# Optimization experiments

Hardware: AMD Instinct MI355X
Metric: run time of the kernel (lower is better)

Reference implementation:

```python
import jax, jax.numpy as jnp
import numpy as np

B = 4194304
RAD2DEG = 180.0 / np.pi


def setup_inputs() -> dict:
    key = jax.random.key(0)
    k1, k2, k3 = jax.random.split(key, 3)
    label = jax.random.normal(k1, (B, 3, 2), dtype=jnp.float32)
    est_label = jax.random.normal(k2, (B, 6), dtype=jnp.float32)
    mix_way = jax.random.randint(k3, (B,), 0, 2, dtype=jnp.int32)  # 0='single', 1=mixed
    return {"label": label, "est_label": est_label, "mix_way": mix_way}


def reference(label, est_label, mix_way):
    # --- permutation-invariant MSE loss ---
    e1, e2 = est_label[:, :3], est_label[:, 3:]            # [B,3] each
    l1, l2 = label[:, :, 0], label[:, :, 1]                 # [B,3] each
    mse = lambda a, b: jnp.mean((a - b) ** 2, axis=-1)      # per-batch mean over 3 comps
    loss_perm1 = mse(e1, l1) + mse(e2, l2)                  # [B]
    loss_perm2 = mse(e2, l1) + mse(e1, l2)                  # [B]
    mixed_loss = jnp.minimum(loss_perm1, loss_perm2)        # [B]
    # 'single' branch in the original uses the FULL (unindexed) tensors -> same scalar each time
    single_loss = jnp.mean((est_label[:, :3] - label[:, :, 0]) ** 2)
    per_batch = jnp.where(mix_way == 0, single_loss, mixed_loss)
    label_loss = jnp.mean(per_batch)

    # --- azimuth MAE with angle wrap-around and best pairing ---
    lab_az1 = jnp.arctan2(label[:, 1, 0], label[:, 0, 0]) * RAD2DEG
    lab_az2 = jnp.arctan2(label[:, 1, 1], label[:, 0, 1]) * RAD2DEG
    est_az1 = jnp.arctan2(est_label[:, 1], est_label[:, 0]) * RAD2DEG
    est_az2 = jnp.arctan2(est_label[:, 4], est_label[:, 3]) * RAD2DEG

    def wrap(e):
        e = jnp.abs(e)
        return jnp.where(e > 180.0, 360.0 - e, e)

    e11 = wrap(lab_az1 - est_az1)
    e22 = wrap(lab_az2 - est_az2)
    e12 = wrap(lab_az1 - est_az2)
    e21 = wrap(lab_az2 - est_az1)

    use_direct = (e11 + e22) < (e12 + e21)
    mae1 = jnp.mean(jnp.where(use_direct, e11, e12))
    mae2 = jnp.mean(jnp.where(use_direct, e22, e21))

    return (label_loss, mae1, mae2)
```

## Files before the change

### kernel.cpp

```cpp
#include <hip/hip_runtime.h>
#include <math.h>

#define RAD2DEG 57.29577951308232f

constexpr int S1_BLOCKS = 2048;
constexpr int S1_TPB    = 256;

__device__ __forceinline__ float wrapdeg(float e) {
    e = fabsf(e);
    return e > 180.0f ? 360.0f - e : e;
}

__device__ __forceinline__ void per_row(
    float l1x, float l2x, float l1y, float l2y, float l1z, float l2z,
    float e1x, float e1y, float e1z, float e2x, float e2y, float e2z,
    int mw,
    float& sS, float& sM, float& sC0, float& sM1, float& sM2)
{
    float dx, dy, dz;
    dx = e1x - l1x; dy = e1y - l1y; dz = e1z - l1z;
    float d11 = dx*dx + dy*dy + dz*dz;
    dx = e2x - l2x; dy = e2y - l2y; dz = e2z - l2z;
    float d22 = dx*dx + dy*dy + dz*dz;
    dx = e2x - l1x; dy = e2y - l1y; dz = e2z - l1z;
    float d21 = dx*dx + dy*dy + dz*dz;
    dx = e1x - l2x; dy = e1y - l2y; dz = e1z - l2z;
    float d12 = dx*dx + dy*dy + dz*dz;

    sS += d11;

    float mixed = fminf(d11 + d22, d21 + d12) * (1.0f / 3.0f);
    if (mw != 0) sM += mixed; else sC0 += 1.0f;

    float la1 = atan2f(l1y, l1x) * RAD2DEG;
    float la2 = atan2f(l2y, l2x) * RAD2DEG;
    float ea1 = atan2f(e1y, e1x) * RAD2DEG;
    float ea2 = atan2f(e2y, e2x) * RAD2DEG;

    float e11 = wrapdeg(la1 - ea1);
    float e22 = wrapdeg(la2 - ea2);
    float e12 = wrapdeg(la1 - ea2);
    float e21 = wrapdeg(la2 - ea1);

    bool ud = (e11 + e22) < (e12 + e21);
    sM1 += ud ? e11 : e12;
    sM2 += ud ? e22 : e21;
}

__global__ __launch_bounds__(S1_TPB) void stage1_kernel(
    const float* __restrict__ label,
    const float* __restrict__ est,
    const int*   __restrict__ mix,
    float* __restrict__ partials,
    int P)
{
    const int tid = threadIdx.x;
    const int gid = blockIdx.x * S1_TPB + tid;
    const int T   = gridDim.x * S1_TPB;

    float sS = 0.f, sM = 0.f, sC0 = 0.f, sM1 = 0.f, sM2 = 0.f;

    for (int p = gid; p < P; p += T) {
        const float4* lab4 = (const float4*)(label + (size_t)p * 12);
        const float4* est4 = (const float4*)(est   + (size_t)p * 12);
        float4 L0 = lab4[0], L1 = lab4[1], L2 = lab4[2];
        float4 E0 = est4[0], E1 = est4[1], E2 = est4[2];
        int2 mw = ((const int2*)mix)[p];

        per_row(L0.x, L0.y, L0.z, L0.w, L1.x, L1.y,
                E0.x, E0.y, E0.z, E0.w, E1.x, E1.y,
                mw.x, sS, sM, sC0, sM1, sM2);
        per_row(L1.z, L1.w, L2.x, L2.y, L2.z, L2.w,
                E1.z, E1.w, E2.x, E2.y, E2.z, E2.w,
                mw.y, sS, sM, sC0, sM1, sM2);
    }

    for (int off = 32; off > 0; off >>= 1) {
        sS  += __shfl_down(sS,  off, 64);
        sM  += __shfl_down(sM,  off, 64);
        sC0 += __shfl_down(sC0, off, 64);
        sM1 += __shfl_down(sM1, off, 64);
        sM2 += __shfl_down(sM2, off, 64);
    }

    __shared__ float red[S1_TPB / 64][5];
    const int wid = tid >> 6, lane = tid & 63;
    if (lane == 0) {
        red[wid][0] = sS; red[wid][1] = sM; red[wid][2] = sC0;
        red[wid][3] = sM1; red[wid][4] = sM2;
    }
    __syncthreads();
    if (tid == 0) {
        float r0 = 0.f, r1 = 0.f, r2 = 0.f, r3 = 0.f, r4 = 0.f;
        #pragma unroll
        for (int w = 0; w < S1_TPB / 64; ++w) {
            r0 += red[w][0]; r1 += red[w][1]; r2 += red[w][2];
            r3 += red[w][3]; r4 += red[w][4];
        }
        float* out = partials + (size_t)blockIdx.x * 5;
        out[0] = r0; out[1] = r1; out[2] = r2; out[3] = r3; out[4] = r4;
    }
}

__global__ __launch_bounds__(256) void stage2_kernel(
    const float* __restrict__ partials,
    float* __restrict__ out,
    int nblocks,
    long long Btot)
{
    const int tid = threadIdx.x;
    double aS = 0, aM = 0, aC0 = 0, aM1 = 0, aM2 = 0;
    for (int r = tid; r < nblocks; r += 256) {
        const float* row = partials + (size_t)r * 5;
        aS += row[0]; aM += row[1]; aC0 += row[2]; aM1 += row[3]; aM2 += row[4];
    }
    for (int off = 32; off > 0; off >>= 1) {
        aS  += __shfl_down(aS,  off, 64);
        aM  += __shfl_down(aM,  off, 64);
        aC0 += __shfl_down(aC0, off, 64);
        aM1 += __shfl_down(aM1, off, 64);
        aM2 += __shfl_down(aM2, off, 64);
    }
    __shared__ double red[4][5];
    const int wid = tid >> 6, lane = tid & 63;
    if (lane == 0) {
        red[wid][0] = aS; red[wid][1] = aM; red[wid][2] = aC0;
        red[wid][3] = aM1; red[wid][4] = aM2;
    }
    __syncthreads();
    if (tid == 0) {
        double S = 0, M = 0, C0 = 0, M1 = 0, M2 = 0;
        #pragma unroll
        for (int w = 0; w < 4; ++w) {
            S += red[w][0]; M += red[w][1]; C0 += red[w][2];
            M1 += red[w][3]; M2 += red[w][4];
        }
        const double Bd = (double)Btot;
        const double single_loss = S / (3.0 * Bd);
        out[0] = (float)((C0 * single_loss + M) / Bd);
        out[1] = (float)(M1 / Bd);
        out[2] = (float)(M2 / Bd);
    }
}

extern "C" void kernel_launch(void* const* d_in, const int* in_sizes, int n_in,
                              void* d_out, int out_size, void* d_ws, size_t ws_size,
                              hipStream_t stream) {
    const float* label = (const float*)d_in[0];
    const float* est   = (const float*)d_in[1];
    const int*   mix   = (const int*)d_in[2];
    float* out = (float*)d_out;
    float* partials = (float*)d_ws;

    const long long B = (long long)in_sizes[2];
    const int P = (int)(B / 2);

    stage1_kernel<<<S1_BLOCKS, S1_TPB, 0, stream>>>(label, est, mix, partials, P);
    stage2_kernel<<<1, 256, 0, stream>>>(partials, out, S1_BLOCKS, B);
}
```

Baseline: 233.2 us.

## Compute wrapped azimuth differences directly via dot/cross polynomial atan

Replaces four atan2f calls and the wrap-around subtraction with a direct angle-between-vectors computation. It uses the dot and cross products of each label/estimate pair, a fast reciprocal and a minimax atan polynomial. This removes the expensive libm atan2 paths, though it now evaluates four angle computations instead of four atan2 calls. The mix-way branch is also turned into a branchless multiply. It risks small accuracy differences from the polynomial and the approximate reciprocal.

```diff
diff --git a/kernel.cpp b/kernel.cpp
--- a/kernel.cpp
+++ b/kernel.cpp
@@ -6,9 +6,24 @@
 constexpr int S1_BLOCKS = 2048;
 constexpr int S1_TPB    = 256;
 
-__device__ __forceinline__ float wrapdeg(float e) {
-    e = fabsf(e);
-    return e > 180.0f ? 360.0f - e : e;
+__device__ __forceinline__ float angdist_deg(float ax, float ay,
+                                             float bx, float by) {
+    float dot = ax * bx + ay * by;
+    float cr  = fabsf(ay * bx - ax * by);
+    float ad  = fabsf(dot);
+    float mn  = fminf(cr, ad);
+    float mx  = fmaxf(cr, ad);
+    float t   = mn * __builtin_amdgcn_rcpf(fmaxf(mx, 1e-37f));
+    float s   = t * t;
+    float p = fmaf(s, -0.01172120f, 0.05265332f);
+    p = fmaf(s, p, -0.11643287f);
+    p = fmaf(s, p,  0.19354346f);
+    p = fmaf(s, p, -0.33262347f);
+    p = fmaf(s, p,  0.99997726f);
+    float a = t * p;
+    a = (cr > ad)    ? (1.57079632679489662f - a) : a;
+    a = (dot < 0.0f) ? (3.14159265358979323f - a) : a;
+    return a * RAD2DEG;
 }
 
 __device__ __forceinline__ void per_row(
@@ -30,17 +45,14 @@
     sS += d11;
 
     float mixed = fminf(d11 + d22, d21 + d12) * (1.0f / 3.0f);
-    if (mw != 0) sM += mixed; else sC0 += 1.0f;
+    float m = (mw != 0) ? 1.0f : 0.0f;
+    sM  += m * mixed;
+    sC0 += 1.0f - m;
 
-    float la1 = atan2f(l1y, l1x) * RAD2DEG;
-    float la2 = atan2f(l2y, l2x) * RAD2DEG;
-    float ea1 = atan2f(e1y, e1x) * RAD2DEG;
-    float ea2 = atan2f(e2y, e2x) * RAD2DEG;
-
-    float e11 = wrapdeg(la1 - ea1);
-    float e22 = wrapdeg(la2 - ea2);
-    float e12 = wrapdeg(la1 - ea2);
-    float e21 = wrapdeg(la2 - ea1);
+    float e11 = angdist_deg(l1x, l1y, e1x, e1y);
+    float e22 = angdist_deg(l2x, l2y, e2x, e2y);
+    float e12 = angdist_deg(l1x, l1y, e2x, e2y);
+    float e21 = angdist_deg(l2x, l2y, e1x, e1y);
 
     bool ud = (e11 + e22) < (e12 + e21);
     sM1 += ud ? e11 : e12;
```

Measured after the change: 231.7 us (median of 2 runs). About the same (-0.6%).
